# Kernel optimization log

Measured on AMD Instinct MI355X. Metric: run time of the kernel, lower is better.

Reference implementation:

```python
import jax, jax.numpy as jnp
import numpy as np

D_MODEL = 1024
NUM_EXPERTS = 16
TOP_K = 2
TOP_C = 4  # min(E, max(4, 2*top_k))
TAU = 1.0
RANK = 64  # max(4, d_model // 16)


def _stable_softmax(v):
    m = jnp.max(v, axis=-1, keepdims=True)
    e = jnp.exp(v - m)
    return e / (jnp.sum(e, axis=-1, keepdims=True) + 1e-12)


def setup_inputs() -> dict:
    key = jax.random.key(0)
    ks = jax.random.split(key, 8)
    B, D, E, R = 16384, D_MODEL, NUM_EXPERTS, RANK
    x = jax.random.normal(ks[0], (B, D), dtype=jnp.float32)
    W_enc = jax.random.normal(ks[1], (D, D), dtype=jnp.float32) * (1.0 / np.sqrt(D))
    b_enc = jnp.zeros((D,), dtype=jnp.float32)
    W_gate = jax.random.normal(ks[2], (E, D), dtype=jnp.float32) * (1.0 / np.sqrt(D))
    U = jax.random.normal(ks[3], (E, R, D), dtype=jnp.float32) * (1.0 / np.sqrt(D))
    V = jax.random.normal(ks[4], (E, D, R), dtype=jnp.float32) * (1.0 / np.sqrt(R))
    gamma = jnp.ones((E,), dtype=jnp.float32)
    return {"x": x, "W_enc": W_enc, "b_enc": b_enc, "W_gate": W_gate,
            "U": U, "V": V, "gamma": gamma}


def reference(x, W_enc, b_enc, W_gate, U, V, gamma):
    # shared encoder
    encoded = x @ W_enc.T + b_enc                      # [B, D]
    # gating: logits -> top_c -> top_k -> softmax over selected logits
    logits = (encoded @ W_gate.T) / TAU                # [B, E]
    topc_vals, topc_idx = jax.lax.top_k(logits, TOP_C)
    topk_vals, pos_in_c = jax.lax.top_k(topc_vals, TOP_K)
    topk_idx = jnp.take_along_axis(topc_idx, pos_in_c, axis=1)  # [B, K]
    topk_w = _stable_softmax(topk_vals)                # [B, K], all > 1e-12
    # dense per-(token, expert) combine weight (equivalent to gather/scatter)
    B = x.shape[0]
    w_dense = jnp.zeros((B, NUM_EXPERTS), dtype=x.dtype)
    w_dense = w_dense.at[jnp.arange(B)[:, None], topk_idx].add(topk_w)
    # low-rank experts: delta_e(x) = gamma_e * silu(x U_e^T) V_e^T
    s = jax.nn.silu(jnp.einsum('bd,erd->ber', encoded, U))        # [B, E, R]
    coef = w_dense * gamma[None, :]                               # [B, E]
    delta = jnp.einsum('ber,edr->bd', s * coef[..., None], V)     # [B, D]
    # y = encoded + sum_k w_k * (expert(x) - x)  with expert(x)-x = delta_e
    return encoded + delta
```

## Files before the change

### kernel.cpp

```cpp
#include <hip/hip_runtime.h>
#include <hip/hip_bf16.h>

#define D_DIM 1024
#define NE 16
#define RK 64
#define NTOK 16384

typedef __bf16 bf16;
typedef __bf16 bf16x8 __attribute__((ext_vector_type(8)));
typedef __bf16 bf16x4 __attribute__((ext_vector_type(4)));
typedef float f32x4 __attribute__((ext_vector_type(4)));

__device__ __forceinline__ void gload16(const void* g, void* l) {
  __builtin_amdgcn_global_load_lds((const __attribute__((address_space(1))) unsigned int*)g,
                                   (__attribute__((address_space(3))) unsigned int*)l,
                                   16, 0, 0);
}

__global__ void k_cast(const float* __restrict__ s, bf16* __restrict__ d, int n4) {
  int i = blockIdx.x * blockDim.x + threadIdx.x;
  if (i >= n4) return;
  float4 v = ((const float4*)s)[i];
  bf16x4 o = { (bf16)v.x, (bf16)v.y, (bf16)v.z, (bf16)v.w };
  ((bf16x4*)d)[i] = o;
}

__global__ void k_castv(const float* __restrict__ V, bf16* __restrict__ Vb2) {
  int id = blockIdx.x * 256 + threadIdx.x;
  int d = id & 1023;
  int rb = (id >> 10) & 7;
  int e = id >> 13;
  const float* src = V + ((size_t)(e * 1024 + d)) * 64 + rb * 8;
  float4 v0 = *(const float4*)src;
  float4 v1 = *(const float4*)(src + 4);
  bf16x8 o = { (bf16)v0.x, (bf16)v0.y, (bf16)v0.z, (bf16)v0.w,
               (bf16)v1.x, (bf16)v1.y, (bf16)v1.z, (bf16)v1.w };
  *(bf16x8*)(Vb2 + (size_t)id * 8) = o;
}

__global__ void k_gmat(const float* __restrict__ Wg, const float* __restrict__ We,
                       float* __restrict__ Gt2) {
  int d = blockIdx.x * 256 + threadIdx.x;
  int e = blockIdx.y;
  int j0 = blockIdx.z * 128;
  double a0 = 0.0, a1 = 0.0, a2 = 0.0, a3 = 0.0;
  for (int j = j0; j < j0 + 128; j += 4) {
    a0 += (double)Wg[e * D_DIM + j + 0] * (double)We[(size_t)(j + 0) * D_DIM + d];
    a1 += (double)Wg[e * D_DIM + j + 1] * (double)We[(size_t)(j + 1) * D_DIM + d];
    a2 += (double)Wg[e * D_DIM + j + 2] * (double)We[(size_t)(j + 2) * D_DIM + d];
    a3 += (double)Wg[e * D_DIM + j + 3] * (double)We[(size_t)(j + 3) * D_DIM + d];
  }
  atomicAdd(&Gt2[(d >> 2) * 64 + e * 4 + (d & 3)], (float)((a0 + a1) + (a2 + a3)));
}

__global__ void k_bgate(const float* __restrict__ Wg, const float* __restrict__ be,
                        float* __restrict__ bg) {
  __shared__ double red[256];
  int e = blockIdx.x, t = threadIdx.x;
  double a = 0.0;
  for (int j = t; j < D_DIM; j += 256) a += (double)Wg[e * D_DIM + j] * (double)be[j];
  red[t] = a; __syncthreads();
  for (int s = 128; s > 0; s >>= 1) { if (t < s) red[t] += red[t + s]; __syncthreads(); }
  if (t == 0) bg[e] = (float)red[0];
}

__global__ __launch_bounds__(256) void k_gatecast(const float* __restrict__ x,
                                                  const float* __restrict__ Gt2,
                                                  const float* __restrict__ bg,
                                                  const float* __restrict__ gamma,
                                                  bf16* __restrict__ xb,
                                                  int* __restrict__ pk,
                                                  float2* __restrict__ wpair) {
  __shared__ float bufx[8][1024];
  __shared__ float Ls[4 * 2 * NE];
  int tid = threadIdx.x;
  int wv = tid >> 6, lane = tid & 63;
  int g = lane & 15;
  int s = lane >> 4;
  int tokbase = blockIdx.x * 8 + wv * 2;

  const float* xr0 = x + (size_t)tokbase * D_DIM;
#pragma unroll
  for (int c = 0; c < 4; ++c) {
    gload16(xr0 + c * 256 + lane * 4, &bufx[wv * 2][c * 256 + lane * 4]);
    gload16(xr0 + D_DIM + c * 256 + lane * 4, &bufx[wv * 2 + 1][c * 256 + lane * 4]);
  }

  const float* Gq = Gt2 + s * 64 + g * 4;
  const float* b0p = &bufx[wv * 2][s * 4];
  const float* b1p = &bufx[wv * 2 + 1][s * 4];
  float acc0 = 0.0f, acc1 = 0.0f;
  float4 gv = *(const float4*)Gq;
  for (int it = 0; it < 64; ++it) {
    int nx = (it < 63) ? it + 1 : 0;
    float4 gn = *(const float4*)(Gq + (size_t)nx * 256);
    float4 x0 = *(const float4*)(b0p + it * 16);
    float4 x1 = *(const float4*)(b1p + it * 16);
    acc0 += x0.x * gv.x + x0.y * gv.y + x0.z * gv.z + x0.w * gv.w;
    acc1 += x1.x * gv.x + x1.y * gv.y + x1.z * gv.z + x1.w * gv.w;
    gv = gn;
  }
  acc0 += __shfl_xor(acc0, 16); acc0 += __shfl_xor(acc0, 32);
  acc1 += __shfl_xor(acc1, 16); acc1 += __shfl_xor(acc1, 32);
  if (s == 0) {
    Ls[wv * 32 + g] = acc0;
    Ls[wv * 32 + 16 + g] = acc1;
  }

#pragma unroll
  for (int t = 0; t < 2; ++t) {
    const float4* src = (const float4*)&bufx[wv * 2 + t][0];
    bf16x4* dst = (bf16x4*)(xb + (size_t)(tokbase + t) * D_DIM);
#pragma unroll
    for (int r = 0; r < 4; ++r) {
      float4 v = src[lane + 64 * r];
      bf16x4 o = { (bf16)v.x, (bf16)v.y, (bf16)v.z, (bf16)v.w };
      dst[lane + 64 * r] = o;
    }
  }
  __syncthreads();

  if (lane < 2) {
    int t = lane;
    int tok = tokbase + t;
    const float* lrow = &Ls[wv * 32 + t * 16];
    float v1 = -1e30f, v2 = -1e30f; int i1 = 0, i2 = 0;
#pragma unroll
    for (int e = 0; e < NE; ++e) {
      float v = lrow[e] + bg[e];
      if (v > v1) { v2 = v1; i2 = i1; v1 = v; i1 = e; }
      else if (v > v2) { v2 = v; i2 = e; }
    }
    float e1 = expf(v2 - v1);
    float den = 1.0f + e1 + 1e-12f;
    float w0 = (1.0f / den) * gamma[i1];
    float w1 = (e1 / den) * gamma[i2];
    pk[tok] = i1 | (i2 << 8);
    wpair[tok] = make_float2(w0, w1);
  }
}

__global__ __launch_bounds__(256) void k_scatter(const int* __restrict__ pk,
                                                 const float2* __restrict__ wpair,
                                                 int* __restrict__ cnt,
                                                 int* __restrict__ lists,
                                                 float* __restrict__ wl) {
  __shared__ int lc[32];
  __shared__ int base[32];
  __shared__ int lc2[32];
  int tid = threadIdx.x;
  int tok = blockIdx.x * 256 + tid;
  if (tid < 32) { lc[tid] = 0; lc2[tid] = 0; }
  __syncthreads();
  int p = pk[tok];
  float2 w = wpair[tok];
  int b0 = p & 0xff;
  int b1 = 16 + ((p >> 8) & 0xff);
  atomicAdd(&lc[b0], 1);
  atomicAdd(&lc[b1], 1);
  __syncthreads();
  if (tid < 32 && lc[tid] > 0) base[tid] = atomicAdd(&cnt[tid], lc[tid]);
  __syncthreads();
  int r0 = base[b0] + atomicAdd(&lc2[b0], 1);
  lists[(size_t)b0 * NTOK + r0] = tok;
  wl[(size_t)b0 * NTOK + r0] = w.x;
  int r1 = base[b1] + atomicAdd(&lc2[b1], 1);
  lists[(size_t)b1 * NTOK + r1] = tok;
  wl[(size_t)b1 * NTOK + r1] = w.y;
}

__global__ void k_btab(const int* __restrict__ cnt, int2* __restrict__ btab,
                       int* __restrict__ nblk) {
  int lane = threadIdx.x;
  int nb = (lane < 32) ? ((cnt[lane] + 63) >> 6) : 0;
  int pfx = nb;
  for (int off = 1; off < 32; off <<= 1) {
    int v = __shfl_up(pfx, off);
    if (lane >= off) pfx += v;
  }
  int start = pfx - nb;
  if (lane < 32) {
    int c = cnt[lane];
    int i = 0;
    for (int t0 = 0; t0 < c; t0 += 64, ++i)
      btab[start + i] = make_int2(lane, t0);
  }
  if (lane == 31) *nblk = pfx;
}

__global__ __launch_bounds__(256) void k_encgemm(const bf16* __restrict__ A,
                                                 const bf16* __restrict__ W,
                                                 const float* __restrict__ bias,
                                                 bf16* __restrict__ encb) {
  __shared__ bf16 As[128 * 64];
  __shared__ bf16 Bs[128 * 64];
  const int K = D_DIM;
  int tid = threadIdx.x;
  int w = blockIdx.x;
  int xcd = w & 7;
  int i = w >> 3;
  int bm = (xcd * 16 + (i & 15)) * 128;
  int bn = (i >> 4) * 128;
  int lane = tid & 63, wv = tid >> 6;
  int wm = (wv >> 1) * 64, wn = (wv & 1) * 64;
  int srow = tid >> 3, scol = (tid & 7) * 8;
  int fr = lane & 15, fk = (lane >> 4) * 8;
  f32x4 acc[4][4] = {};
  for (int k0 = 0; k0 < K; k0 += 64) {
    __syncthreads();
#pragma unroll
    for (int p = 0; p < 4; ++p) {
      int r = p * 32 + srow;
      gload16(A + (size_t)(bm + r) * K + k0 + scol, &As[r * 64 + scol]);
    }
#pragma unroll
    for (int p = 0; p < 4; ++p) {
      int r = p * 32 + srow;
      gload16(W + (size_t)(bn + r) * K + k0 + scol, &Bs[r * 64 + scol]);
    }
    __syncthreads();
#pragma unroll
    for (int kk = 0; kk < 2; ++kk) {
      bf16x8 af[4], bv[4];
#pragma unroll
      for (int m = 0; m < 4; ++m)
        af[m] = *(const bf16x8*)&As[(wm + m * 16 + fr) * 64 + kk * 32 + fk];
#pragma unroll
      for (int n = 0; n < 4; ++n)
        bv[n] = *(const bf16x8*)&Bs[(wn + n * 16 + fr) * 64 + kk * 32 + fk];
#pragma unroll
      for (int m = 0; m < 4; ++m)
#pragma unroll
        for (int n = 0; n < 4; ++n)
          acc[m][n] = __builtin_amdgcn_mfma_f32_16x16x32_bf16(af[m], bv[n], acc[m][n], 0, 0, 0);
    }
  }
  int rg = (lane >> 4) * 4;
#pragma unroll
  for (int n = 0; n < 4; ++n) {
    int col = bn + wn + n * 16 + fr;
    float bval = bias[col];
#pragma unroll
    for (int m = 0; m < 4; ++m) {
#pragma unroll
      for (int r = 0; r < 4; ++r) {
        int row = bm + wm + m * 16 + rg + r;
        encb[(size_t)row * D_DIM + col] = (bf16)(acc[m][n][r] + bval);
      }
    }
  }
}

__global__ __launch_bounds__(256) void k_expert(const bf16* __restrict__ encb,
                                                const bf16* __restrict__ Ub,
                                                const bf16* __restrict__ Vb2,
                                                const int* __restrict__ cnt,
                                                const int* __restrict__ lists,
                                                const float* __restrict__ wl,
                                                const int2* __restrict__ btab,
                                                const int* __restrict__ nblk,
                                                bf16* __restrict__ d0,
                                                bf16* __restrict__ d1) {
  int bid = blockIdx.x;
  if (bid >= *nblk) return;
  int2 bt = btab[bid];
  int bin = bt.x, t0 = bt.y;
  int slot = bin >> 4, e = bin & 15;
  int c = cnt[bin];
  int nrows = c - t0; if (nrows > 64) nrows = 64;
  const int* tl = lists + (size_t)bin * NTOK + t0;
  const float* wlp = wl + (size_t)bin * NTOK + t0;

  __shared__ int toks[64];
  __shared__ float coefs[64];
  __shared__ bf16 As[64 * 64];
  __shared__ bf16 Us[64 * 64];
  __shared__ bf16 Ss[64 * 64];

  int tid = threadIdx.x;
  if (tid < 64) {
    int rr = tid < nrows ? tid : nrows - 1;
    toks[tid] = tl[rr];
    coefs[tid] = tid < nrows ? wlp[tid] : 0.0f;
  }
  __syncthreads();

  int lane = tid & 63, wv = tid >> 6;
  int srow = tid >> 3, scol = (tid & 7) * 8;
  int fr = lane & 15, fk = (lane >> 4) * 8;
  size_t tokA0 = (size_t)toks[srow] * D_DIM;
  size_t tokA1 = (size_t)toks[32 + srow] * D_DIM;
  const bf16* Ue = Ub + (size_t)e * RK * D_DIM;
  f32x4 acc1[4] = {};

  for (int k0 = 0; k0 < D_DIM; k0 += 64) {
    __syncthreads();
    gload16(encb + tokA0 + k0 + scol, &As[srow * 64 + scol]);
    gload16(encb + tokA1 + k0 + scol, &As[(32 + srow) * 64 + scol]);
    gload16(Ue + (size_t)srow * D_DIM + k0 + scol, &Us[srow * 64 + scol]);
    gload16(Ue + (size_t)(32 + srow) * D_DIM + k0 + scol, &Us[(32 + srow) * 64 + scol]);
    __syncthreads();
#pragma unroll
    for (int kk = 0; kk < 2; ++kk) {
      bf16x8 af = *(const bf16x8*)&As[(wv * 16 + fr) * 64 + kk * 32 + fk];
#pragma unroll
      for (int n = 0; n < 4; ++n) {
        bf16x8 bv = *(const bf16x8*)&Us[(n * 16 + fr) * 64 + kk * 32 + fk];
        acc1[n] = __builtin_amdgcn_mfma_f32_16x16x32_bf16(af, bv, acc1[n], 0, 0, 0);
      }
    }
  }
  int rg = (lane >> 4) * 4;
#pragma unroll
  for (int n = 0; n < 4; ++n)
#pragma unroll
    for (int r = 0; r < 4; ++r) {
      int row = wv * 16 + rg + r;
      float v = acc1[n][r];
      float s = v / (1.0f + __expf(-v));
      Ss[row * 64 + n * 16 + fr] = (bf16)(s * coefs[row]);
    }
  __syncthreads();
  bf16x8 a2[4][2];
#pragma unroll
  for (int m = 0; m < 4; ++m)
#pragma unroll
    for (int kk = 0; kk < 2; ++kk)
      a2[m][kk] = *(const bf16x8*)&Ss[(m * 16 + fr) * 64 + kk * 32 + fk];

  const bf16* Ve2 = Vb2 + (size_t)e * RK * D_DIM;
  bf16* dst = slot ? d1 : d0;
  int rb0 = lane >> 4;
  int colbase = wv * 256;
  for (int nj = 0; nj < 16; ++nj) {
    int dcol = colbase + nj * 16 + fr;
    bf16x8 b0 = *(const bf16x8*)&Ve2[((size_t)rb0 * D_DIM + dcol) * 8];
    bf16x8 b1 = *(const bf16x8*)&Ve2[((size_t)(rb0 + 4) * D_DIM + dcol) * 8];
#pragma unroll
    for (int m = 0; m < 4; ++m) {
      f32x4 a = {};
      a = __builtin_amdgcn_mfma_f32_16x16x32_bf16(a2[m][0], b0, a, 0, 0, 0);
      a = __builtin_amdgcn_mfma_f32_16x16x32_bf16(a2[m][1], b1, a, 0, 0, 0);
#pragma unroll
      for (int r = 0; r < 4; ++r) {
        int row = m * 16 + rg + r;
        if (row < nrows) {
          dst[(size_t)toks[row] * D_DIM + dcol] = (bf16)a[r];
        }
      }
    }
  }
}

__global__ __launch_bounds__(256) void k_final(float* __restrict__ out,
                                               const bf16* __restrict__ encb,
                                               const bf16* __restrict__ d0,
                                               const bf16* __restrict__ d1) {
  size_t i = ((size_t)blockIdx.x * 256 + threadIdx.x) * 8;
  bf16x8 e = *(const bf16x8*)(encb + i);
  bf16x8 a = *(const bf16x8*)(d0 + i);
  bf16x8 b = *(const bf16x8*)(d1 + i);
  float4 o0, o1;
  o0.x = (float)e[0] + (float)a[0] + (float)b[0];
  o0.y = (float)e[1] + (float)a[1] + (float)b[1];
  o0.z = (float)e[2] + (float)a[2] + (float)b[2];
  o0.w = (float)e[3] + (float)a[3] + (float)b[3];
  o1.x = (float)e[4] + (float)a[4] + (float)b[4];
  o1.y = (float)e[5] + (float)a[5] + (float)b[5];
  o1.z = (float)e[6] + (float)a[6] + (float)b[6];
  o1.w = (float)e[7] + (float)a[7] + (float)b[7];
  *(float4*)(out + i) = o0;
  *(float4*)(out + i + 4) = o1;
}

extern "C" void kernel_launch(void* const* d_in, const int* in_sizes, int n_in,
                              void* d_out, int out_size, void* d_ws, size_t ws_size,
                              hipStream_t stream) {
  const float* x   = (const float*)d_in[0];
  const float* We  = (const float*)d_in[1];
  const float* be  = (const float*)d_in[2];
  const float* Wg  = (const float*)d_in[3];
  const float* U   = (const float*)d_in[4];
  const float* V   = (const float*)d_in[5];
  const float* gam = (const float*)d_in[6];
  float* out = (float*)d_out;
  char* ws = (char*)d_ws;

  int*    cnt  = (int*)(ws + 0);
  float*  Gt2  = (float*)(ws + 256);
  float*  bg   = (float*)(ws + 66048);
  int2*   btab = (int2*)(ws + 66176);
  int*    nblk = (int*)(ws + 70656);
  bf16*   xb   = (bf16*)(ws + 131072);
  bf16*   d0   = (bf16*)(ws + 131072);
  bf16*   encb = (bf16*)(ws + 131072 + 33554432);
  char*   base = ws + 131072 + 2 * 33554432;
  bf16*   Wb   = (bf16*)(base);
  bf16*   Ubf  = (bf16*)(base + 2097152);
  bf16*   Vb2  = (bf16*)(base + 2 * 2097152);
  int*    lists= (int*)(base + 3 * 2097152);
  float*  wl   = (float*)(base + 4 * 2097152);
  int*    pk   = (int*)(base + 5 * 2097152);
  float2* wpr  = (float2*)(base + 5 * 2097152 + 131072);
  bf16*   d1   = (bf16*)(base + 5 * 2097152 + 131072 + 131072 + 131072);

  hipMemsetAsync(ws, 0, 66048, stream);

  k_cast<<<1024, 256, 0, stream>>>(We, Wb, 1048576 / 4);
  k_cast<<<1024, 256, 0, stream>>>(U, Ubf, 1048576 / 4);
  k_castv<<<512, 256, 0, stream>>>(V, Vb2);

  dim3 gg(4, 16, 8);
  k_gmat<<<gg, 256, 0, stream>>>(Wg, We, Gt2);
  k_bgate<<<16, 256, 0, stream>>>(Wg, be, bg);

  k_gatecast<<<2048, 256, 0, stream>>>(x, Gt2, bg, gam, xb, pk, wpr);
  k_scatter<<<64, 256, 0, stream>>>(pk, wpr, cnt, lists, wl);
  k_btab<<<1, 64, 0, stream>>>(cnt, btab, nblk);

  k_encgemm<<<1024, 256, 0, stream>>>(xb, Wb, be, encb);

  k_expert<<<544, 256, 0, stream>>>(encb, Ubf, Vb2, cnt, lists, wl, btab, nblk, d0, d1);
  k_final<<<8192, 256, 0, stream>>>(out, encb, d0, d1);
}
```

Measured before the change: 189.9 us.

## Enlarge encoder GEMM tiles to 256x256 with XOR-swizzled LDS layout

The encoder GEMM moves from 128x128 tiles with 4 waves to 256x256 tiles with 8 waves, each wave computing a 128x64 sub-tile. Shared-memory rows are XOR-swizzled by row index to avoid bank conflicts on fragment reads. This raises operand reuse per block and cuts global/L2 traffic, and drops the XCD-aware block remapping. In exchange the grid shrinks to 256 blocks, roughly one per CU at a single block per CU. Register pressure also rises with 32 accumulators per wave, and there is still no double buffering.

Result: faster. 183.8 us (-3.2%).

```diff
diff --git a/kernel.cpp b/kernel.cpp
--- a/kernel.cpp
+++ b/kernel.cpp
@@ -188,48 +188,51 @@
   if (lane == 31) *nblk = pfx;
 }
 
-__global__ __launch_bounds__(256) void k_encgemm(const bf16* __restrict__ A,
-                                                 const bf16* __restrict__ W,
-                                                 const float* __restrict__ bias,
-                                                 bf16* __restrict__ encb) {
-  __shared__ bf16 As[128 * 64];
-  __shared__ bf16 Bs[128 * 64];
-  const int K = D_DIM;
+__global__ __launch_bounds__(512, 1) void k_encgemm(const bf16* __restrict__ A,
+                                                    const bf16* __restrict__ W,
+                                                    const float* __restrict__ bias,
+                                                    bf16* __restrict__ encb) {
+  __shared__ bf16 As[256 * 64];
+  __shared__ bf16 Bs[256 * 64];
   int tid = threadIdx.x;
   int w = blockIdx.x;
-  int xcd = w & 7;
-  int i = w >> 3;
-  int bm = (xcd * 16 + (i & 15)) * 128;
-  int bn = (i >> 4) * 128;
+  int bm = (w & 63) * 256;
+  int bn = (w >> 6) * 256;
   int lane = tid & 63, wv = tid >> 6;
-  int wm = (wv >> 1) * 64, wn = (wv & 1) * 64;
-  int srow = tid >> 3, scol = (tid & 7) * 8;
+  int wm = (wv >> 2) * 128, wn = (wv & 3) * 64;
+  int srow = tid >> 3;
+  int sc = tid & 7;
+  int cs = sc ^ (srow & 7);
   int fr = lane & 15, fk = (lane >> 4) * 8;
-  f32x4 acc[4][4] = {};
-  for (int k0 = 0; k0 < K; k0 += 64) {
+  f32x4 acc[8][4] = {};
+  for (int k0 = 0; k0 < D_DIM; k0 += 64) {
     __syncthreads();
 #pragma unroll
     for (int p = 0; p < 4; ++p) {
-      int r = p * 32 + srow;
-      gload16(A + (size_t)(bm + r) * K + k0 + scol, &As[r * 64 + scol]);
+      int r = p * 64 + srow;
+      gload16(A + (size_t)(bm + r) * D_DIM + k0 + cs * 8, &As[r * 64 + sc * 8]);
     }
 #pragma unroll
     for (int p = 0; p < 4; ++p) {
-      int r = p * 32 + srow;
-      gload16(W + (size_t)(bn + r) * K + k0 + scol, &Bs[r * 64 + scol]);
+      int r = p * 64 + srow;
+      gload16(W + (size_t)(bn + r) * D_DIM + k0 + cs * 8, &Bs[r * 64 + sc * 8]);
     }
     __syncthreads();
 #pragma unroll
     for (int kk = 0; kk < 2; ++kk) {
-      bf16x8 af[4], bv[4];
-#pragma unroll
-      for (int m = 0; m < 4; ++m)
-        af[m] = *(const bf16x8*)&As[(wm + m * 16 + fr) * 64 + kk * 32 + fk];
-#pragma unroll
-      for (int n = 0; n < 4; ++n)
-        bv[n] = *(const bf16x8*)&Bs[(wn + n * 16 + fr) * 64 + kk * 32 + fk];
-#pragma unroll
-      for (int m = 0; m < 4; ++m)
+      bf16x8 af[8], bv[4];
+#pragma unroll
+      for (int m = 0; m < 8; ++m) {
+        int row = wm + m * 16 + fr;
+        af[m] = *(const bf16x8*)&As[(row * 64 + kk * 32 + fk) ^ ((row & 7) << 3)];
+      }
+#pragma unroll
+      for (int n = 0; n < 4; ++n) {
+        int row = wn + n * 16 + fr;
+        bv[n] = *(const bf16x8*)&Bs[(row * 64 + kk * 32 + fk) ^ ((row & 7) << 3)];
+      }
+#pragma unroll
+      for (int m = 0; m < 8; ++m)
 #pragma unroll
         for (int n = 0; n < 4; ++n)
           acc[m][n] = __builtin_amdgcn_mfma_f32_16x16x32_bf16(af[m], bv[n], acc[m][n], 0, 0, 0);
@@ -241,7 +244,7 @@
     int col = bn + wn + n * 16 + fr;
     float bval = bias[col];
 #pragma unroll
-    for (int m = 0; m < 4; ++m) {
+    for (int m = 0; m < 8; ++m) {
 #pragma unroll
       for (int r = 0; r < 4; ++r) {
         int row = bm + wm + m * 16 + rg + r;
@@ -418,7 +421,7 @@
   k_scatter<<<64, 256, 0, stream>>>(pk, wpr, cnt, lists, wl);
   k_btab<<<1, 64, 0, stream>>>(cnt, btab, nblk);
 
-  k_encgemm<<<1024, 256, 0, stream>>>(xb, Wb, be, encb);
+  k_encgemm<<<256, 512, 0, stream>>>(xb, Wb, be, encb);
 
   k_expert<<<544, 256, 0, stream>>>(encb, Ubf, Vb2, cnt, lists, wl, btab, nblk, d0, d1);
   k_final<<<8192, 256, 0, stream>>>(out, encb, d0, d1);
```
